# Optimization experiments

Hardware: AMD Instinct MI355X
Metric: run time of the kernel (lower is better)

## Reference

```python
import jax, jax.numpy as jnp
import numpy as np

ALPHA = 0.3

def setup_inputs() -> dict:
    key = jax.random.key(0)
    k1, k2, k3, k4 = jax.random.split(key, 4)
    bz, sl, n_pos = 64, 1024, 50
    a_arc = jax.random.normal(k1, (bz, sl, sl), dtype=jnp.float32)
    s_arc = jax.random.normal(k2, (bz, sl, sl), dtype=jnp.float32)
    adds = jax.random.randint(k3, (bz, sl), 0, n_pos, dtype=jnp.int32)
    pos = jax.random.randint(k4, (bz, sl), 0, n_pos, dtype=jnp.int32)
    return {"a_arc": a_arc, "s_arc": s_arc, "adds": adds, "pos": pos, "n_pos": n_pos}


def reference(a_arc, s_arc, adds, pos, n_pos):
    # Bin index for every (head, dep) pair: bin = adds[b,i]*n_pos + adds[b,j]
    bins_add = adds[:, :, None] * n_pos + adds[:, None, :]          # [bz, sl, sl] int32
    # Histogram: sum a_arc values per POS-pair bin (replaces the O(n_pos^2) masked loop)
    score_arc = jax.ops.segment_sum(
        a_arc.reshape(-1), bins_add.reshape(-1), num_segments=n_pos * n_pos)
    score_arc = jax.nn.sigmoid(score_arc)                            # [n_pos^2]
    # Broadcast the binned scores back onto s_arc via the pos-pair bins
    bins_pos = pos[:, :, None] * n_pos + pos[:, None, :]             # [bz, sl, sl]
    return s_arc + ALPHA * score_arc[bins_pos]
```

## Files before the change

### kernel.cpp

```cpp
#include <hip/hip_runtime.h>

constexpr int NPOS  = 50;
constexpr int NBINS = NPOS * NPOS;
constexpr int SL    = 1024;
constexpr int BZ    = 64;
constexpr float ALPHA = 0.3f;

constexpr int H_THREADS  = 256;
constexpr int COLCHUNKS  = 4;
constexpr int ROWSPLITS  = 2;
constexpr int H_ROWS     = SL / ROWSPLITS;
constexpr int H_BLOCKS   = BZ * COLCHUNKS * ROWSPLITS;

constexpr int A_THREADS       = 256;
constexpr int ROWS_PER_BLOCK  = 32;
constexpr int BLOCKS_PER_B    = SL / ROWS_PER_BLOCK;
constexpr int A_BLOCKS        = BZ * BLOCKS_PER_B;

__global__ __launch_bounds__(H_THREADS) void hist_kernel(
    const float* __restrict__ a, const int* __restrict__ adds,
    float* __restrict__ g_hist) {
  __shared__ float accL[NPOS][H_THREADS];
  __shared__ int   adds_s[SL];
  __shared__ int   cnt2[NPOS];
  __shared__ int   off2s[NPOS];
  __shared__ int   off2m[NPOS];
  __shared__ int   order2[H_THREADS];

  const int tid    = threadIdx.x;
  const int b      = blockIdx.x / (COLCHUNKS * ROWSPLITS);
  const int rem    = blockIdx.x % (COLCHUNKS * ROWSPLITS);
  const int cc     = rem / ROWSPLITS;
  const int rsplit = rem % ROWSPLITS;
  const int i0     = rsplit * H_ROWS;

  ((int4*)adds_s)[tid] = ((const int4*)(adds + (size_t)b * SL))[tid];
  #pragma unroll
  for (int p = 0; p < NPOS; ++p) accL[p][tid] = 0.0f;
  if (tid < NPOS) cnt2[tid] = 0;
  __syncthreads();

  const int j = cc * H_THREADS + tid;
  const int q = adds_s[j];

  const float* __restrict__ P = a + ((size_t)b * SL + i0) * SL + j;
  for (int r0 = 0; r0 < H_ROWS; r0 += 16) {
    float v[16];
    #pragma unroll
    for (int k = 0; k < 16; ++k)
      v[k] = P[(size_t)(r0 + k) * SL];
    int bs[16];
    #pragma unroll
    for (int k4 = 0; k4 < 4; ++k4) {
      const int4 b4 = *(const int4*)&adds_s[i0 + r0 + k4 * 4];
      bs[k4 * 4 + 0] = b4.x; bs[k4 * 4 + 1] = b4.y;
      bs[k4 * 4 + 2] = b4.z; bs[k4 * 4 + 3] = b4.w;
    }
    #pragma unroll
    for (int k = 0; k < 16; ++k)
      accL[bs[k]][tid] += v[k];
  }

  atomicAdd(&cnt2[q], 1);
  __syncthreads();
  if (tid == 0) {
    int run = 0;
    for (int c = 0; c < NPOS; ++c) { off2s[c] = run; off2m[c] = run; run += cnt2[c]; }
  }
  __syncthreads();
  order2[atomicAdd(&off2m[q], 1)] = tid;
  __syncthreads();

  for (int bin = tid; bin < NBINS; bin += H_THREADS) {
    const int p  = bin / NPOS;
    const int qq = bin % NPOS;
    const int s0 = off2s[qq];
    const int n  = cnt2[qq];
    float s = 0.0f;
    for (int k = 0; k < n; ++k) s += accL[p][order2[s0 + k]];
    atomicAdd(&g_hist[bin], s);
  }
}

__global__ __launch_bounds__(A_THREADS) void apply_kernel(
    const float* __restrict__ s, const int* __restrict__ pos,
    const float* __restrict__ g_hist, float* __restrict__ out) {
  __shared__ float sig[NBINS];
  __shared__ int   pos_s[SL];

  const int tid = threadIdx.x;
  const int b   = blockIdx.x / BLOCKS_PER_B;
  const int i0  = (blockIdx.x % BLOCKS_PER_B) * ROWS_PER_BLOCK;

  ((int4*)pos_s)[tid] = ((const int4*)(pos + (size_t)b * SL))[tid];
  for (int k = tid; k < NBINS; k += A_THREADS) {
    const float h = g_hist[k];
    sig[k] = 1.0f / (1.0f + __expf(-h));
  }
  __syncthreads();

  const int4 pj = ((const int4*)pos_s)[tid];
  const size_t rowoff = ((size_t)b * SL + i0) * SL;
  const float4* __restrict__ srow = (const float4*)(s + rowoff);
  float4* __restrict__ orow = (float4*)(out + rowoff);

  for (int r = 0; r < ROWS_PER_BLOCK; ++r) {
    const int base = pos_s[i0 + r] * NPOS;
    const float4 sv = srow[(size_t)r * (SL / 4) + tid];
    float4 ov;
    ov.x = sv.x + ALPHA * sig[base + pj.x];
    ov.y = sv.y + ALPHA * sig[base + pj.y];
    ov.z = sv.z + ALPHA * sig[base + pj.z];
    ov.w = sv.w + ALPHA * sig[base + pj.w];
    orow[(size_t)r * (SL / 4) + tid] = ov;
  }
}

extern "C" void kernel_launch(void* const* d_in, const int* in_sizes, int n_in,
                              void* d_out, int out_size, void* d_ws, size_t ws_size,
                              hipStream_t stream) {
  const float* a_arc = (const float*)d_in[0];
  const float* s_arc = (const float*)d_in[1];
  const int*   adds  = (const int*)d_in[2];
  const int*   pos   = (const int*)d_in[3];
  float* out    = (float*)d_out;
  float* g_hist = (float*)d_ws;

  hipMemsetAsync(g_hist, 0, NBINS * sizeof(float), stream);

  hist_kernel <<<H_BLOCKS, H_THREADS, 0, stream>>>(a_arc, adds, g_hist);
  apply_kernel<<<A_BLOCKS, A_THREADS, 0, stream>>>(s_arc, pos, g_hist, out);
}
```

Baseline: 188.5 us.

## Process two columns per thread with float2 loads and double-buffered row batches

The histogram kernel now uses 128 threads, each handling two adjacent columns. It loads them as float2 and keeps two shared accumulator arrays, one for even and one for odd columns. The row loop is software-pipelined with two register buffers, so the next 16-row batch of global loads is issued before the current batch's shared-memory read-modify-writes. This aims to raise memory-level parallelism and halve load instruction count. In exchange it uses more registers and LDS per block, and the final reduction has a branchy even/odd lookup.

Result: no change. 190.2 us (+0.9%).

```diff
diff --git a/kernel.cpp b/kernel.cpp
--- a/kernel.cpp
+++ b/kernel.cpp
@@ -6,11 +6,12 @@
 constexpr int BZ    = 64;
 constexpr float ALPHA = 0.3f;
 
-constexpr int H_THREADS  = 256;
-constexpr int COLCHUNKS  = 4;
-constexpr int ROWSPLITS  = 2;
-constexpr int H_ROWS     = SL / ROWSPLITS;
-constexpr int H_BLOCKS   = BZ * COLCHUNKS * ROWSPLITS;
+constexpr int H_THREADS = 128;
+constexpr int H_COLS    = 2 * H_THREADS;
+constexpr int COLCHUNKS = SL / H_COLS;
+constexpr int ROWSPLITS = 2;
+constexpr int H_ROWS    = SL / ROWSPLITS;
+constexpr int H_BLOCKS  = BZ * COLCHUNKS * ROWSPLITS;
 
 constexpr int A_THREADS       = 256;
 constexpr int ROWS_PER_BLOCK  = 32;
@@ -20,12 +21,13 @@
 __global__ __launch_bounds__(H_THREADS) void hist_kernel(
     const float* __restrict__ a, const int* __restrict__ adds,
     float* __restrict__ g_hist) {
-  __shared__ float accL[NPOS][H_THREADS];
+  __shared__ float accA[NPOS][H_THREADS];
+  __shared__ float accB[NPOS][H_THREADS];
   __shared__ int   adds_s[SL];
   __shared__ int   cnt2[NPOS];
   __shared__ int   off2s[NPOS];
   __shared__ int   off2m[NPOS];
-  __shared__ int   order2[H_THREADS];
+  __shared__ int   order2[H_COLS];
 
   const int tid    = threadIdx.x;
   const int b      = blockIdx.x / (COLCHUNKS * ROWSPLITS);
@@ -34,41 +36,63 @@
   const int rsplit = rem % ROWSPLITS;
   const int i0     = rsplit * H_ROWS;
 
-  ((int4*)adds_s)[tid] = ((const int4*)(adds + (size_t)b * SL))[tid];
+  {
+    const int4* src = (const int4*)(adds + (size_t)b * SL);
+    ((int4*)adds_s)[tid]             = src[tid];
+    ((int4*)adds_s)[tid + H_THREADS] = src[tid + H_THREADS];
+  }
   #pragma unroll
-  for (int p = 0; p < NPOS; ++p) accL[p][tid] = 0.0f;
+  for (int p = 0; p < NPOS; ++p) { accA[p][tid] = 0.0f; accB[p][tid] = 0.0f; }
   if (tid < NPOS) cnt2[tid] = 0;
   __syncthreads();
 
-  const int j = cc * H_THREADS + tid;
-  const int q = adds_s[j];
+  const int j0 = cc * H_COLS + 2 * tid;
+  const int q0 = adds_s[j0];
+  const int q1 = adds_s[j0 + 1];
 
-  const float* __restrict__ P = a + ((size_t)b * SL + i0) * SL + j;
-  for (int r0 = 0; r0 < H_ROWS; r0 += 16) {
-    float v[16];
+  const float2* __restrict__ P =
+      (const float2*)(a + ((size_t)b * SL + i0) * SL + j0);
+  constexpr int RSTRIDE = SL / 2;
+
+  auto loadset = [&](float2 (&v)[16], int (&bs)[16], int R0) {
     #pragma unroll
     for (int k = 0; k < 16; ++k)
-      v[k] = P[(size_t)(r0 + k) * SL];
-    int bs[16];
+      v[k] = P[(size_t)(R0 + k) * RSTRIDE];
     #pragma unroll
     for (int k4 = 0; k4 < 4; ++k4) {
-      const int4 b4 = *(const int4*)&adds_s[i0 + r0 + k4 * 4];
+      const int4 b4 = *(const int4*)&adds_s[i0 + R0 + k4 * 4];
       bs[k4 * 4 + 0] = b4.x; bs[k4 * 4 + 1] = b4.y;
       bs[k4 * 4 + 2] = b4.z; bs[k4 * 4 + 3] = b4.w;
     }
+  };
+  auto rmwset = [&](float2 (&v)[16], int (&bs)[16]) {
     #pragma unroll
-    for (int k = 0; k < 16; ++k)
-      accL[bs[k]][tid] += v[k];
+    for (int k = 0; k < 16; ++k) {
+      accA[bs[k]][tid] += v[k].x;
+      accB[bs[k]][tid] += v[k].y;
+    }
+  };
+
+  float2 v0[16], v1[16];
+  int    bs0[16], bs1[16];
+  loadset(v0, bs0, 0);
+  for (int r0 = 0; r0 < H_ROWS; r0 += 32) {
+    loadset(v1, bs1, r0 + 16);
+    rmwset(v0, bs0);
+    if (r0 + 32 < H_ROWS) loadset(v0, bs0, r0 + 32);
+    rmwset(v1, bs1);
   }
 
-  atomicAdd(&cnt2[q], 1);
+  atomicAdd(&cnt2[q0], 1);
+  atomicAdd(&cnt2[q1], 1);
   __syncthreads();
   if (tid == 0) {
     int run = 0;
     for (int c = 0; c < NPOS; ++c) { off2s[c] = run; off2m[c] = run; run += cnt2[c]; }
   }
   __syncthreads();
-  order2[atomicAdd(&off2m[q], 1)] = tid;
+  order2[atomicAdd(&off2m[q0], 1)] = 2 * tid;
+  order2[atomicAdd(&off2m[q1], 1)] = 2 * tid + 1;
   __syncthreads();
 
   for (int bin = tid; bin < NBINS; bin += H_THREADS) {
@@ -77,7 +101,10 @@
     const int s0 = off2s[qq];
     const int n  = cnt2[qq];
     float s = 0.0f;
-    for (int k = 0; k < n; ++k) s += accL[p][order2[s0 + k]];
+    for (int k = 0; k < n; ++k) {
+      const int c = order2[s0 + k];
+      s += (c & 1) ? accB[p][c >> 1] : accA[p][c >> 1];
+    }
     atomicAdd(&g_hist[bin], s);
   }
 }
```
